# Optimization experiments

Measured on AMD Instinct MI355X. Metric: run time of the kernel, lower is better.

## Reference

```python
import jax, jax.numpy as jnp
import numpy as np

DIM = 512
H = 8          # num_heads
C = 64         # dim_head
HID = H * C    # 512
NMEM = H       # num_mem_kv = num_heads


def _rmsnorm_seq(x, w):
    # F.normalize(x, dim=2) * w * sqrt(dim)
    n = jnp.sqrt(jnp.sum(x * x, axis=2, keepdims=True))
    return x / jnp.maximum(n, 1e-12) * w * jnp.asarray(DIM ** 0.5, x.dtype)


def setup_inputs() -> dict:
    key = jax.random.key(0)
    ks = jax.random.split(key, 7)
    b, n = 4, 4096
    x = jax.random.normal(ks[0], (b, n, DIM), dtype=jnp.float32)
    norm_w = jnp.ones((1, 1, DIM), dtype=jnp.float32)
    w_qkv = jax.random.normal(ks[1], (DIM, 3 * HID), dtype=jnp.float32) / np.sqrt(DIM)
    mem_kv = jax.random.normal(ks[2], (2, H, C, NMEM), dtype=jnp.float32)
    w_out = jax.random.normal(ks[3], (HID, DIM), dtype=jnp.float32) / np.sqrt(HID)
    b_out = jax.random.normal(ks[4], (DIM,), dtype=jnp.float32) * 0.01
    out_norm_w = jnp.ones((1, 1, DIM), dtype=jnp.float32)
    return {"x": x, "norm_w": norm_w, "w_qkv": w_qkv, "mem_kv": mem_kv,
            "w_out": w_out, "b_out": b_out, "out_norm_w": out_norm_w}


def reference(x, norm_w, w_qkv, mem_kv, w_out, b_out, out_norm_w):
    b, n, _ = x.shape
    scale = jnp.asarray(C ** -0.5, x.dtype)
    xn = _rmsnorm_seq(x, norm_w)
    qkv = xn @ w_qkv                                   # [b, n, 3*HID]
    q, k, v = jnp.split(qkv, 3, axis=2)
    # b n (h c) -> b h c n
    def to_heads(t):
        return t.reshape(b, n, H, C).transpose(0, 2, 3, 1)
    q, k, v = map(to_heads, (q, k, v))                 # [b, H, C, n]
    mk = jnp.broadcast_to(mem_kv[0], (b, H, C, NMEM))
    mv = jnp.broadcast_to(mem_kv[1], (b, H, C, NMEM))
    k = jnp.concatenate([mk, k], axis=-1)              # [b, H, C, n+NMEM]
    v = jnp.concatenate([mv, v], axis=-1)
    q = jax.nn.softmax(q, axis=-2) * scale             # softmax over feature dim c
    k = jax.nn.softmax(k, axis=-1)                     # softmax over token dim n
    context = jnp.einsum('bhdn,bhen->bhde', k, v)      # [b, H, C, C]
    out = jnp.einsum('bhde,bhdn->bhen', context, q)    # [b, H, C, n]
    out = out.transpose(0, 3, 1, 2).reshape(b, n, HID)  # b h c n -> b n (h c)
    out = out @ w_out + b_out
    return _rmsnorm_seq(out, out_norm_w)
```

## Files before the change

kernel.cpp:

```cpp
#include <hip/hip_runtime.h>
#include <hip/hip_bf16.h>


typedef __attribute__((ext_vector_type(8))) __bf16 bf16x8;
typedef __attribute__((ext_vector_type(4))) __bf16 bf16x4;
typedef __attribute__((ext_vector_type(4))) float f32x4;

#define SQRT_DIM 22.627416997969522f

__device__ __forceinline__ void gload_lds16(const void* g, void* l) {
  __builtin_amdgcn_global_load_lds((__attribute__((address_space(1))) void*)g,
                                   (__attribute__((address_space(3))) void*)l, 16, 0, 0);
}

__global__ __launch_bounds__(256) void pre_k(const float* __restrict__ x,
                                             const float* __restrict__ nw,
                                             __bf16* __restrict__ xn,
                                             const float* __restrict__ wqkv,
                                             __bf16* __restrict__ WqkvT) {
  __shared__ float tbuf[64][65];
  const int bid = blockIdx.x;
  const int tid = threadIdx.x;
  if (bid < 4096) {
    const int row = bid * 4 + (tid >> 6);
    const int lane = tid & 63;
    const float4* xr = (const float4*)(x + (size_t)row * 512);
    float4 v0 = xr[lane], v1 = xr[lane + 64];
    float s = v0.x * v0.x + v0.y * v0.y + v0.z * v0.z + v0.w * v0.w +
              v1.x * v1.x + v1.y * v1.y + v1.z * v1.z + v1.w * v1.w;
#pragma unroll
    for (int m = 1; m < 64; m <<= 1) s += __shfl_xor(s, m);
    const float sc = SQRT_DIM / fmaxf(sqrtf(s), 1e-12f);
    const float4* wr4 = (const float4*)nw;
    float4 w0 = wr4[lane], w1 = wr4[lane + 64];
    __bf16* o = xn + (size_t)row * 512;
    bf16x4 a, b2;
    a[0] = (__bf16)(v0.x * sc * w0.x); a[1] = (__bf16)(v0.y * sc * w0.y);
    a[2] = (__bf16)(v0.z * sc * w0.z); a[3] = (__bf16)(v0.w * sc * w0.w);
    b2[0] = (__bf16)(v1.x * sc * w1.x); b2[1] = (__bf16)(v1.y * sc * w1.y);
    b2[2] = (__bf16)(v1.z * sc * w1.z); b2[3] = (__bf16)(v1.w * sc * w1.w);
    *(bf16x4*)(o + lane * 4) = a;
    *(bf16x4*)(o + 256 + lane * 4) = b2;
  } else {
    const int t = bid - 4096;
    const int bx = t % 24, by = t / 24;
    const int n0 = bx * 64, k0 = by * 64;
    const int r = tid >> 4, c4 = (tid & 15) * 4;
#pragma unroll
    for (int p = 0; p < 4; ++p) {
      float4 v = *(const float4*)(wqkv + (size_t)(k0 + p * 16 + r) * 1536 + n0 + c4);
      tbuf[p * 16 + r][c4 + 0] = v.x;
      tbuf[p * 16 + r][c4 + 1] = v.y;
      tbuf[p * 16 + r][c4 + 2] = v.z;
      tbuf[p * 16 + r][c4 + 3] = v.w;
    }
    __syncthreads();
    const int base = (n0 < 512) ? n0
                     : (n0 < 1024 ? 512 + ((n0 - 512) >> 6) * 128
                                  : 512 + ((n0 - 1024) >> 6) * 128 + 64);
#pragma unroll
    for (int p = 0; p < 4; ++p) {
      int c = p * 256 + tid;
      int rn = c >> 4, cc = (c & 15) * 4;
      bf16x4 o;
#pragma unroll
      for (int j = 0; j < 4; ++j) o[j] = (__bf16)tbuf[cc + j][rn];
      *(bf16x4*)(WqkvT + (size_t)(base + rn) * 512 + k0 + cc) = o;
    }
  }
}

__global__ __launch_bounds__(256) void gemm1_k(const __bf16* __restrict__ A,
                                               const __bf16* __restrict__ BT,
                                               __bf16* __restrict__ QS,
                                               float* __restrict__ pctx,
                                               float* __restrict__ pden) {
  __shared__ __align__(16) char smem[65536];
  const int K = 512;
  const int NT = 8;
  const int NX = 12;
  const int tid = threadIdx.x;
  const int lane = tid & 63;
  const int wave = tid >> 6;
  const int wr = (wave >> 1) * 64;
  const int wc = (wave & 1) * 64;
  const int l15 = lane & 15, lg = lane >> 4;
  const int cpx = gridDim.x >> 3;
  const int fid = blockIdx.x;
  const int tile = (fid & 7) * cpx + (fid >> 3);
  const int my = tile / NX;
  const int m0 = my * 128;
  const int n0 = (tile - my * NX) * 128;
  const int sw0 = lg ^ (l15 & 7);
  const int sw1 = (4 + lg) ^ (l15 & 7);

  f32x4 acc[4][4] = {};

  auto stage = [&](int buf, int k0) {
#pragma unroll
    for (int it = 0; it < 4; ++it) {
      int flat = it * 256 + tid;
      int row = flat >> 3;
      int cb = ((flat & 7) ^ (row & 7)) * 16;
      gload_lds16((const char*)(A + (size_t)(m0 + row) * K + k0) + cb,
                  smem + buf * 16384 + flat * 16);
    }
#pragma unroll
    for (int it = 0; it < 4; ++it) {
      int flat = it * 256 + tid;
      int row = flat >> 3;
      int cb = ((flat & 7) ^ (row & 7)) * 16;
      gload_lds16((const char*)(BT + (size_t)(n0 + row) * K + k0) + cb,
                  smem + 32768 + buf * 16384 + flat * 16);
    }
  };

  stage(0, 0);
  stage(1, 64);
  asm volatile("s_waitcnt vmcnt(8)" ::: "memory");
  __builtin_amdgcn_s_barrier();

  for (int kt = 0; kt < NT; ++kt) {
    const int cur = kt & 1;
    const __bf16* Asb = (const __bf16*)(smem + cur * 16384);
    const __bf16* Bsb = (const __bf16*)(smem + 32768 + cur * 16384);
    bf16x8 a0[4], b0[4], a1[4], b1[4];
#pragma unroll
    for (int i = 0; i < 4; ++i) {
      a0[i] = *(const bf16x8*)(&Asb[(wr + i * 16 + l15) * 64 + sw0 * 8]);
      b0[i] = *(const bf16x8*)(&Bsb[(wc + i * 16 + l15) * 64 + sw0 * 8]);
      a1[i] = *(const bf16x8*)(&Asb[(wr + i * 16 + l15) * 64 + sw1 * 8]);
      b1[i] = *(const bf16x8*)(&Bsb[(wc + i * 16 + l15) * 64 + sw1 * 8]);
    }
    asm volatile("s_waitcnt lgkmcnt(0)" ::: "memory");
    __builtin_amdgcn_sched_barrier(0);
    __builtin_amdgcn_s_barrier();
    if (kt + 2 < NT) stage(cur, (kt + 2) * 64);
    __builtin_amdgcn_s_setprio(1);
#pragma unroll
    for (int mi = 0; mi < 4; ++mi)
#pragma unroll
      for (int ni = 0; ni < 4; ++ni)
        acc[mi][ni] = __builtin_amdgcn_mfma_f32_16x16x32_bf16(a0[mi], b0[ni],
                                                              acc[mi][ni], 0, 0, 0);
    __builtin_amdgcn_s_setprio(0);
    __builtin_amdgcn_s_setprio(1);
#pragma unroll
    for (int mi = 0; mi < 4; ++mi)
#pragma unroll
      for (int ni = 0; ni < 4; ++ni)
        acc[mi][ni] = __builtin_amdgcn_mfma_f32_16x16x32_bf16(a1[mi], b1[ni],
                                                              acc[mi][ni], 0, 0, 0);
    __builtin_amdgcn_s_setprio(0);
    if (kt < NT - 1) {
      if (kt + 2 < NT)
        asm volatile("s_waitcnt vmcnt(8)" ::: "memory");
      else
        asm volatile("s_waitcnt vmcnt(0)" ::: "memory");
      __builtin_amdgcn_s_barrier();
    }
  }

  if (n0 < 512) {
    __bf16* Cs = (__bf16*)smem;
#pragma unroll
    for (int mi = 0; mi < 4; ++mi)
#pragma unroll
      for (int r = 0; r < 4; ++r) {
        float v0_ = acc[mi][0][r], v1_ = acc[mi][1][r], v2_ = acc[mi][2][r],
              v3_ = acc[mi][3][r];
        float mx = fmaxf(fmaxf(v0_, v1_), fmaxf(v2_, v3_));
#pragma unroll
        for (int m = 1; m < 16; m <<= 1) mx = fmaxf(mx, __shfl_xor(mx, m));
        float e0 = __expf(v0_ - mx), e1 = __expf(v1_ - mx),
              e2 = __expf(v2_ - mx), e3 = __expf(v3_ - mx);
        float s = e0 + e1 + e2 + e3;
#pragma unroll
        for (int m = 1; m < 16; m <<= 1) s += __shfl_xor(s, m);
        float inv = 0.125f / s;
        int row = wr + mi * 16 + lg * 4 + r;
        Cs[row * 132 + wc + l15] = (__bf16)(e0 * inv);
        Cs[row * 132 + wc + 16 + l15] = (__bf16)(e1 * inv);
        Cs[row * 132 + wc + 32 + l15] = (__bf16)(e2 * inv);
        Cs[row * 132 + wc + 48 + l15] = (__bf16)(e3 * inv);
      }
    __syncthreads();
    const int sr = tid >> 4, sc = tid & 15;
#pragma unroll
    for (int p = 0; p < 8; ++p) {
      int row = p * 16 + sr;
      bf16x8 v = *(const bf16x8*)(&Cs[row * 132 + sc * 8]);
      *(bf16x8*)(QS + (size_t)(m0 + row) * 512 + n0 + sc * 8) = v;
    }
  } else {
    const int h = (n0 >> 7) - 4;
    __bf16* EKs = (__bf16*)smem;
    __bf16* Vs = (__bf16*)(smem + 17408);
#pragma unroll
    for (int mi = 0; mi < 4; ++mi) {
      const int tok0 = wr + mi * 16 + lg * 4;
#pragma unroll
      for (int ni = 0; ni < 4; ++ni) {
        int c = wc + ni * 16 + l15;
        bf16x4 p;
        if (wc == 0) {
#pragma unroll
          for (int r = 0; r < 4; ++r) p[r] = (__bf16)__expf(acc[mi][ni][r]);
          *(bf16x4*)(&EKs[c * 136 + tok0]) = p;
        } else {
#pragma unroll
          for (int r = 0; r < 4; ++r) p[r] = (__bf16)acc[mi][ni][r];
          *(bf16x4*)(&Vs[(c - 64) * 136 + tok0]) = p;
        }
      }
    }
    __syncthreads();
    const int b = m0 >> 12, chunk = (m0 & 4095) >> 7;
    const int wg = (b * 8 + h) * 32 + chunk;
    if (tid < 64) {
      float s = 0.0f;
#pragma unroll
      for (int t8 = 0; t8 < 16; ++t8) {
        bf16x8 v = *(const bf16x8*)(&EKs[tid * 136 + t8 * 8]);
#pragma unroll
        for (int j = 0; j < 8; ++j) s += (float)v[j];
      }
      pden[(size_t)wg * 64 + tid] = s;
    }
    f32x4 cacc[2][2] = {};
#pragma unroll
    for (int kt = 0; kt < 4; ++kt) {
      bf16x8 afr[2], bfr[2];
#pragma unroll
      for (int i = 0; i < 2; ++i) {
        int d = ((wave >> 1) * 2 + i) * 16 + l15;
        afr[i] = *(const bf16x8*)(&EKs[d * 136 + kt * 32 + lg * 8]);
        int e = ((wave & 1) * 2 + i) * 16 + l15;
        bfr[i] = *(const bf16x8*)(&Vs[e * 136 + kt * 32 + lg * 8]);
      }
#pragma unroll
      for (int i = 0; i < 2; ++i)
#pragma unroll
        for (int j = 0; j < 2; ++j)
          cacc[i][j] = __builtin_amdgcn_mfma_f32_16x16x32_bf16(afr[i], bfr[j],
                                                               cacc[i][j], 0, 0, 0);
    }
    float* op = pctx + (size_t)wg * 4096;
#pragma unroll
    for (int i = 0; i < 2; ++i)
#pragma unroll
      for (int j = 0; j < 2; ++j) {
        int e = ((wave & 1) * 2 + j) * 16 + l15;
#pragma unroll
        for (int r = 0; r < 4; ++r) {
          int d = ((wave >> 1) * 2 + i) * 16 + lg * 4 + r;
          op[d * 64 + e] = cacc[i][j][r];
        }
      }
  }
}

__global__ __launch_bounds__(512) void gemm2rms(const __bf16* __restrict__ QS,
                                                const __bf16* __restrict__ W2T,
                                                const float* __restrict__ bias,
                                                const float* __restrict__ onw,
                                                float* __restrict__ out) {
  __shared__ __bf16 As[2][64 * 64];
  __shared__ __bf16 Bs[2][512 * 64];
  __shared__ float rss[64][8];
  const int K = 512;
  const int NT = 8;
  const int tid = threadIdx.x;
  const int lane = tid & 63;
  const int wave = tid >> 6;
  const int wc = wave * 64;
  const int l15 = lane & 15, lg = lane >> 4;
  const int cpx = gridDim.x >> 3;
  const int fid = blockIdx.x;
  const int tile = (fid & 7) * cpx + (fid >> 3);
  const int m0 = tile * 64;
  const __bf16* bt = W2T + (size_t)(m0 >> 12) * 262144;

  f32x4 acc[4][4] = {};

  auto stage = [&](int buf, int k0) {
    {
      int flat = tid;
      int row = flat >> 3;
      int cb = ((flat & 7) ^ (row & 7)) * 16;
      gload_lds16((const char*)(QS + (size_t)(m0 + row) * K + k0) + cb,
                  (char*)(&As[buf][0]) + flat * 16);
    }
#pragma unroll
    for (int it = 0; it < 8; ++it) {
      int flat = it * 512 + tid;
      int row = flat >> 3;
      int cb = ((flat & 7) ^ (row & 7)) * 16;
      gload_lds16((const char*)(bt + (size_t)row * K + k0) + cb,
                  (char*)(&Bs[buf][0]) + flat * 16);
    }
  };

  stage(0, 0);
  stage(1, 64);
  asm volatile("s_waitcnt vmcnt(9)" ::: "memory");
  __builtin_amdgcn_s_barrier();

  for (int kt = 0; kt < NT; ++kt) {
    const int cur = kt & 1;
    bf16x8 a0[4], b0[4], a1[4], b1[4];
    const int sw0 = lg ^ (l15 & 7);
    const int sw1 = (4 + lg) ^ (l15 & 7);
#pragma unroll
    for (int i = 0; i < 4; ++i) {
      a0[i] = *(const bf16x8*)(&As[cur][(i * 16 + l15) * 64 + sw0 * 8]);
      b0[i] = *(const bf16x8*)(&Bs[cur][(wc + i * 16 + l15) * 64 + sw0 * 8]);
      a1[i] = *(const bf16x8*)(&As[cur][(i * 16 + l15) * 64 + sw1 * 8]);
      b1[i] = *(const bf16x8*)(&Bs[cur][(wc + i * 16 + l15) * 64 + sw1 * 8]);
    }
    asm volatile("s_waitcnt lgkmcnt(0)" ::: "memory");
    __builtin_amdgcn_sched_barrier(0);
    __builtin_amdgcn_s_barrier();
    if (kt + 2 < NT) stage(cur, (kt + 2) * 64);
    __builtin_amdgcn_s_setprio(1);
#pragma unroll
    for (int mi = 0; mi < 4; ++mi)
#pragma unroll
      for (int ni = 0; ni < 4; ++ni)
        acc[mi][ni] = __builtin_amdgcn_mfma_f32_16x16x32_bf16(a0[mi], b0[ni],
                                                              acc[mi][ni], 0, 0, 0);
    __builtin_amdgcn_s_setprio(0);
    __builtin_amdgcn_s_setprio(1);
#pragma unroll
    for (int mi = 0; mi < 4; ++mi)
#pragma unroll
      for (int ni = 0; ni < 4; ++ni)
        acc[mi][ni] = __builtin_amdgcn_mfma_f32_16x16x32_bf16(a1[mi], b1[ni],
                                                              acc[mi][ni], 0, 0, 0);
    __builtin_amdgcn_s_setprio(0);
    if (kt < NT - 1) {
      if (kt + 2 < NT)
        asm volatile("s_waitcnt vmcnt(9)" ::: "memory");
      else
        asm volatile("s_waitcnt vmcnt(0)" ::: "memory");
      __builtin_amdgcn_s_barrier();
    }
  }

  float bv[4], wv[4];
#pragma unroll
  for (int ni = 0; ni < 4; ++ni) {
    int col = wc + ni * 16 + l15;
    bv[ni] = bias[col];
    wv[ni] = onw[col];
  }
  float vv[4][4][4];
#pragma unroll
  for (int mi = 0; mi < 4; ++mi)
#pragma unroll
    for (int ni = 0; ni < 4; ++ni)
#pragma unroll
      for (int r = 0; r < 4; ++r) vv[mi][ni][r] = acc[mi][ni][r] + bv[ni];
#pragma unroll
  for (int mi = 0; mi < 4; ++mi)
#pragma unroll
    for (int r = 0; r < 4; ++r) {
      float ps = vv[mi][0][r] * vv[mi][0][r] + vv[mi][1][r] * vv[mi][1][r] +
                 vv[mi][2][r] * vv[mi][2][r] + vv[mi][3][r] * vv[mi][3][r];
#pragma unroll
      for (int m = 1; m < 16; m <<= 1) ps += __shfl_xor(ps, m);
      if (l15 == 0) rss[mi * 16 + lg * 4 + r][wave] = ps;
    }
  __syncthreads();
#pragma unroll
  for (int mi = 0; mi < 4; ++mi)
#pragma unroll
    for (int r = 0; r < 4; ++r) {
      int row = mi * 16 + lg * 4 + r;
      float ss = rss[row][0] + rss[row][1] + rss[row][2] + rss[row][3] +
                 rss[row][4] + rss[row][5] + rss[row][6] + rss[row][7];
      float sc = SQRT_DIM / fmaxf(sqrtf(ss), 1e-12f);
      size_t rb = (size_t)(m0 + row) * 512;
#pragma unroll
      for (int ni = 0; ni < 4; ++ni)
        out[rb + wc + ni * 16 + l15] = vv[mi][ni][r] * sc * wv[ni];
    }
}

__global__ __launch_bounds__(256) void ctx_final(const float* __restrict__ pctx,
                                                 const float* __restrict__ pden,
                                                 const float* __restrict__ memkv,
                                                 float* __restrict__ ctx) {
  const int bh = blockIdx.x >> 3, dg = blockIdx.x & 7;
  const int h = bh & 7;
  const int tid = threadIdx.x;
  __shared__ float sden[8][9];
  if (tid < 64) {
    const int dl = tid >> 3, part = tid & 7;
    const int d = dg * 8 + dl;
    float s = 0.0f;
#pragma unroll
    for (int c = 0; c < 4; ++c)
      s += pden[((size_t)bh * 32 + part * 4 + c) * 64 + d];
    if (part == 0) {
#pragma unroll
      for (int m = 0; m < 8; ++m)
        s += __expf(memkv[(size_t)h * 512 + d * 8 + m]);
    }
    sden[dl][part] = s;
  }
  __syncthreads();
  const int dl = tid >> 5, e2 = (tid & 31) * 2;
  const int d = dg * 8 + dl;
  float den = sden[dl][0] + sden[dl][1] + sden[dl][2] + sden[dl][3] +
              sden[dl][4] + sden[dl][5] + sden[dl][6] + sden[dl][7];
  float invd = 1.0f / den;
  float s0 = 0.0f, s1 = 0.0f;
#pragma unroll
  for (int m = 0; m < 8; ++m) {
    float ek = __expf(memkv[(size_t)h * 512 + d * 8 + m]);
    s0 += ek * memkv[4096 + (size_t)h * 512 + e2 * 8 + m];
    s1 += ek * memkv[4096 + (size_t)h * 512 + (e2 + 1) * 8 + m];
  }
#pragma unroll
  for (int c = 0; c < 32; ++c) {
    float2 p = *(const float2*)(pctx + ((size_t)bh * 32 + c) * 4096 + d * 64 + e2);
    s0 += p.x;
    s1 += p.y;
  }
  float2 o = make_float2(s0 * invd, s1 * invd);
  *(float2*)(ctx + (size_t)bh * 4096 + d * 64 + e2) = o;
}

__global__ __launch_bounds__(256) void make_w2t(const float* __restrict__ ctx,
                                                const float* __restrict__ wout,
                                                __bf16* __restrict__ W2T) {
  const int wg = blockIdx.x;
  const int b = wg >> 6, h = (wg >> 3) & 7, jc = wg & 7;
  const int j0 = jc * 64;
  const int tid = threadIdx.x;
  __shared__ float cs[64][65];
  __shared__ float wo[64][64];
  const float* ch = ctx + ((size_t)b * 8 + h) * 4096;
#pragma unroll
  for (int it = 0; it < 16; ++it) {
    int flat = it * 256 + tid;
    cs[flat >> 6][flat & 63] = ch[flat];
  }
#pragma unroll
  for (int it = 0; it < 16; ++it) {
    int flat = it * 256 + tid;
    int e = flat >> 6, j = flat & 63;
    wo[e][j] = wout[(size_t)(h * 64 + e) * 512 + j0 + j];
  }
  __syncthreads();
  const int d = tid & 63;
  const int jg = (tid >> 6) * 16;
  for (int jj = 0; jj < 16; ++jj) {
    int j = jg + jj;
    float s = 0.0f;
#pragma unroll
    for (int e = 0; e < 64; ++e) s += cs[d][e] * wo[e][j];
    W2T[(size_t)b * 262144 + (size_t)(j0 + j) * 512 + h * 64 + d] = (__bf16)s;
  }
}

extern "C" void kernel_launch(void* const* d_in, const int* in_sizes, int n_in,
                              void* d_out, int out_size, void* d_ws, size_t ws_size,
                              hipStream_t stream) {
  const float* x = (const float*)d_in[0];
  const float* norm_w = (const float*)d_in[1];
  const float* w_qkv = (const float*)d_in[2];
  const float* mem_kv = (const float*)d_in[3];
  const float* w_out = (const float*)d_in[4];
  const float* b_out = (const float*)d_in[5];
  const float* onw = (const float*)d_in[6];

  char* ws = (char*)d_ws;
  __bf16* xn = (__bf16*)(ws + 0);
  __bf16* WqkvT = (__bf16*)(ws + 16777216);
  float* pctx = (float*)(ws + 18350080);
  __bf16* QS = (__bf16*)(ws + 51904512);
  float* pden = (float*)(ws + 68681728);
  float* ctx = (float*)(ws + 68943872);
  __bf16* W2T = (__bf16*)(ws + 69468160);

  pre_k<<<4288, 256, 0, stream>>>(x, norm_w, xn, w_qkv, WqkvT);
  gemm1_k<<<1536, 256, 0, stream>>>(xn, WqkvT, QS, pctx, pden);
  ctx_final<<<256, 256, 0, stream>>>(pctx, pden, mem_kv, ctx);
  make_w2t<<<256, 256, 0, stream>>>(ctx, w_out, W2T);
  gemm2rms<<<256, 512, 0, stream>>>(QS, W2T, b_out, onw, (float*)d_out);
}
```

Before: 88.41 us.

## Reduce per-chunk context partials with atomics and fuse ctx finalize into W2T build

The GEMM1 kernel now accumulates each chunk's context and denominator partials into one per-(batch, head) buffer with global float atomicAdd, instead of writing 32 separate partial slices. The ctx_final kernel is removed, and its memory-KV contribution and normalisation move into the W2T construction kernel, with a memset added to zero the accumulators. This removes a kernel launch and the large partial-buffer write and read. In exchange it adds atomic contention (32 chunks per address), a memset launch, and summation order that is no longer deterministic.

Measured after the change: 91.22 us. 1.03x slower.

```diff
diff --git a/kernel.cpp b/kernel.cpp
--- a/kernel.cpp
+++ b/kernel.cpp
@@ -73,8 +73,8 @@
 __global__ __launch_bounds__(256) void gemm1_k(const __bf16* __restrict__ A,
                                                const __bf16* __restrict__ BT,
                                                __bf16* __restrict__ QS,
-                                               float* __restrict__ pctx,
-                                               float* __restrict__ pden) {
+                                               float* __restrict__ ctxsum,
+                                               float* __restrict__ den) {
   __shared__ __align__(16) char smem[65536];
   const int K = 512;
   const int NT = 8;
@@ -215,8 +215,8 @@
       }
     }
     __syncthreads();
-    const int b = m0 >> 12, chunk = (m0 & 4095) >> 7;
-    const int wg = (b * 8 + h) * 32 + chunk;
+    const int b = m0 >> 12;
+    const int bh = b * 8 + h;
     if (tid < 64) {
       float s = 0.0f;
 #pragma unroll
@@ -225,7 +225,7 @@
 #pragma unroll
         for (int j = 0; j < 8; ++j) s += (float)v[j];
       }
-      pden[(size_t)wg * 64 + tid] = s;
+      atomicAdd(&den[(size_t)bh * 64 + tid], s);
     }
     f32x4 cacc[2][2] = {};
 #pragma unroll
@@ -245,7 +245,7 @@
           cacc[i][j] = __builtin_amdgcn_mfma_f32_16x16x32_bf16(afr[i], bfr[j],
                                                                cacc[i][j], 0, 0, 0);
     }
-    float* op = pctx + (size_t)wg * 4096;
+    float* cp = ctxsum + (size_t)bh * 4096;
 #pragma unroll
     for (int i = 0; i < 2; ++i)
 #pragma unroll
@@ -254,7 +254,7 @@
 #pragma unroll
         for (int r = 0; r < 4; ++r) {
           int d = ((wave >> 1) * 2 + i) * 16 + lg * 4 + r;
-          op[d * 64 + e] = cacc[i][j][r];
+          atomicAdd(&cp[d * 64 + e], cacc[i][j][r]);
         }
       }
   }
@@ -387,65 +387,40 @@
     }
 }
 
-__global__ __launch_bounds__(256) void ctx_final(const float* __restrict__ pctx,
-                                                 const float* __restrict__ pden,
-                                                 const float* __restrict__ memkv,
-                                                 float* __restrict__ ctx) {
-  const int bh = blockIdx.x >> 3, dg = blockIdx.x & 7;
-  const int h = bh & 7;
-  const int tid = threadIdx.x;
-  __shared__ float sden[8][9];
-  if (tid < 64) {
-    const int dl = tid >> 3, part = tid & 7;
-    const int d = dg * 8 + dl;
-    float s = 0.0f;
-#pragma unroll
-    for (int c = 0; c < 4; ++c)
-      s += pden[((size_t)bh * 32 + part * 4 + c) * 64 + d];
-    if (part == 0) {
-#pragma unroll
-      for (int m = 0; m < 8; ++m)
-        s += __expf(memkv[(size_t)h * 512 + d * 8 + m]);
-    }
-    sden[dl][part] = s;
-  }
-  __syncthreads();
-  const int dl = tid >> 5, e2 = (tid & 31) * 2;
-  const int d = dg * 8 + dl;
-  float den = sden[dl][0] + sden[dl][1] + sden[dl][2] + sden[dl][3] +
-              sden[dl][4] + sden[dl][5] + sden[dl][6] + sden[dl][7];
-  float invd = 1.0f / den;
-  float s0 = 0.0f, s1 = 0.0f;
-#pragma unroll
-  for (int m = 0; m < 8; ++m) {
-    float ek = __expf(memkv[(size_t)h * 512 + d * 8 + m]);
-    s0 += ek * memkv[4096 + (size_t)h * 512 + e2 * 8 + m];
-    s1 += ek * memkv[4096 + (size_t)h * 512 + (e2 + 1) * 8 + m];
-  }
-#pragma unroll
-  for (int c = 0; c < 32; ++c) {
-    float2 p = *(const float2*)(pctx + ((size_t)bh * 32 + c) * 4096 + d * 64 + e2);
-    s0 += p.x;
-    s1 += p.y;
-  }
-  float2 o = make_float2(s0 * invd, s1 * invd);
-  *(float2*)(ctx + (size_t)bh * 4096 + d * 64 + e2) = o;
-}
-
-__global__ __launch_bounds__(256) void make_w2t(const float* __restrict__ ctx,
-                                                const float* __restrict__ wout,
-                                                __bf16* __restrict__ W2T) {
+__global__ __launch_bounds__(256) void ctxw2t(const float* __restrict__ ctxsum,
+                                              const float* __restrict__ den,
+                                              const float* __restrict__ memkv,
+                                              const float* __restrict__ wout,
+                                              __bf16* __restrict__ W2T) {
   const int wg = blockIdx.x;
   const int b = wg >> 6, h = (wg >> 3) & 7, jc = wg & 7;
+  const int bh = b * 8 + h;
   const int j0 = jc * 64;
   const int tid = threadIdx.x;
   __shared__ float cs[64][65];
   __shared__ float wo[64][64];
-  const float* ch = ctx + ((size_t)b * 8 + h) * 4096;
+  __shared__ float emk[64][8], mvl[64][8], invd[64];
+  if (tid < 64) {
+    float dsum = den[(size_t)bh * 64 + tid];
+#pragma unroll
+    for (int m = 0; m < 8; ++m) {
+      float e = __expf(memkv[(size_t)h * 512 + tid * 8 + m]);
+      emk[tid][m] = e;
+      dsum += e;
+      mvl[tid][m] = memkv[4096 + (size_t)h * 512 + tid * 8 + m];
+    }
+    invd[tid] = 1.0f / dsum;
+  }
+  __syncthreads();
+  const float* ch = ctxsum + (size_t)bh * 4096;
 #pragma unroll
   for (int it = 0; it < 16; ++it) {
     int flat = it * 256 + tid;
-    cs[flat >> 6][flat & 63] = ch[flat];
+    int d = flat >> 6, e = flat & 63;
+    float s = ch[flat];
+#pragma unroll
+    for (int m = 0; m < 8; ++m) s += emk[d][m] * mvl[e][m];
+    cs[d][e] = s * invd[d];
   }
 #pragma unroll
   for (int it = 0; it < 16; ++it) {
@@ -479,15 +454,14 @@
   char* ws = (char*)d_ws;
   __bf16* xn = (__bf16*)(ws + 0);
   __bf16* WqkvT = (__bf16*)(ws + 16777216);
-  float* pctx = (float*)(ws + 18350080);
   __bf16* QS = (__bf16*)(ws + 51904512);
-  float* pden = (float*)(ws + 68681728);
-  float* ctx = (float*)(ws + 68943872);
+  float* den = (float*)(ws + 68681728);
+  float* ctxsum = (float*)(ws + 68943872);
   __bf16* W2T = (__bf16*)(ws + 69468160);
 
+  hipMemsetAsync(ws + 68681728, 0, 786432, stream);
   pre_k<<<4288, 256, 0, stream>>>(x, norm_w, xn, w_qkv, WqkvT);
-  gemm1_k<<<1536, 256, 0, stream>>>(xn, WqkvT, QS, pctx, pden);
-  ctx_final<<<256, 256, 0, stream>>>(pctx, pden, mem_kv, ctx);
-  make_w2t<<<256, 256, 0, stream>>>(ctx, w_out, W2T);
+  gemm1_k<<<1536, 256, 0, stream>>>(xn, WqkvT, QS, ctxsum, den);
+  ctxw2t<<<256, 256, 0, stream>>>(ctxsum, den, mem_kv, w_out, W2T);
   gemm2rms<<<256, 512, 0, stream>>>(QS, W2T, b_out, onw, (float*)d_out);
 }
```
